# Kernel tuning notes

Hardware: AMD Instinct MI355X
Metric: run time of the kernel (lower is better)

The kernel has to match this reference:

```python
import jax, jax.numpy as jnp
import numpy as np

HEADS = 12
D_MODEL = 768
D_K = D_MODEL // HEADS


def setup_inputs() -> dict:
    key = jax.random.key(0)
    ks = jax.random.split(key, 5)
    B, S = 2, 2048
    scale = 1.0 / np.sqrt(D_MODEL)
    return {
        "q": jax.random.normal(ks[0], (B, S, D_MODEL), dtype=jnp.float32),
        "k": jax.random.normal(ks[1], (B, S, D_MODEL), dtype=jnp.float32),
        "v": jax.random.normal(ks[2], (B, S, D_MODEL), dtype=jnp.float32),
        "Wk": jax.random.normal(ks[3], (D_MODEL, D_MODEL), dtype=jnp.float32) * scale,
        "bk": jnp.zeros((D_MODEL,), dtype=jnp.float32),
        "Wo": jax.random.normal(ks[4], (D_MODEL, D_MODEL), dtype=jnp.float32) * scale,
        "bo": jnp.zeros((D_MODEL,), dtype=jnp.float32),
    }


def reference(q, k, v, Wk, bk, Wo, bo):
    B, S, _ = q.shape
    # NOTE: faithful to source bug: q, k, v ALL projected with k_linear.
    def proj(x):
        y = x @ Wk.T + bk                    # [B,S,D]
        return y.reshape(B, -1, HEADS, D_K).transpose(0, 2, 1, 3)  # [B,H,S,Dk]

    qh, kh, vh = proj(q), proj(k), proj(v)
    scores = jnp.einsum('bhsd,bhtd->bhst', qh, kh) / jnp.sqrt(jnp.float32(D_K))
    attn = jax.nn.softmax(scores, axis=-1)   # dropout is identity in eval
    out = jnp.einsum('bhst,bhtd->bhsd', attn, vh)
    concat = out.transpose(0, 2, 1, 3).reshape(B, -1, D_MODEL)
    return concat @ Wo.T + bo
```

## Files before the change

kernel.cpp:

```cpp
#include <hip/hip_runtime.h>
#include <hip/hip_bf16.h>
#include <stddef.h>

#define HEADS 12
#define DM 768
#define DK 64
#define SEQ 2048
#define NB 2
#define WSZ (DM * DM)

typedef __attribute__((ext_vector_type(8))) short short8;
typedef __attribute__((ext_vector_type(4))) float f32x4;

#define MFMA16(A, B, C) __builtin_amdgcn_mfma_f32_16x16x32_bf16((A), (B), (C), 0, 0, 0)

__device__ __forceinline__ unsigned short f2bf(float x) {
  union { float f; unsigned u; } c;
  c.f = x;
  unsigned r = (c.u + 0x7FFFu + ((c.u >> 16) & 1u)) >> 16;
  return (unsigned short)r;
}
__device__ __forceinline__ float bf2f(unsigned short h) {
  union { float f; unsigned u; } c;
  c.u = ((unsigned)h) << 16;
  return c.f;
}

__device__ __forceinline__ void async16(const void* g, void* l) {
  __builtin_amdgcn_global_load_lds(
      (const __attribute__((address_space(1))) void*)g,
      (__attribute__((address_space(3))) void*)l, 16, 0, 0);
}

__device__ __forceinline__ void splitpk(float a, float b, unsigned& hu, unsigned& lu) {
  union { __hip_bfloat162 v; unsigned u; } c;
  c.v = __float22bfloat162_rn(make_float2(a, b));
  hu = c.u;
  const float ra = a - bf2f((unsigned short)(hu & 0xFFFFu));
  const float rb = b - bf2f((unsigned short)(hu >> 16));
  c.v = __float22bfloat162_rn(make_float2(ra, rb));
  lu = c.u;
}

__device__ __forceinline__ unsigned pk2bf(float a, float b) {
  union { __hip_bfloat162 v; unsigned u; } c;
  c.v = __float22bfloat162_rn(make_float2(a, b));
  return c.u;
}

__global__ __launch_bounds__(256) void prep_split(
    const float* __restrict__ q, const float* __restrict__ k,
    const float* __restrict__ v, const float* __restrict__ Wk,
    const float* __restrict__ Wo, unsigned short* __restrict__ xq_h,
    unsigned short* __restrict__ xq_l, unsigned short* __restrict__ xk_h,
    unsigned short* __restrict__ xv_h, unsigned short* __restrict__ wkh,
    unsigned short* __restrict__ wkl, unsigned short* __restrict__ woh,
    unsigned short* __restrict__ wol) {
  const int id = blockIdx.x;
  const float* S;
  unsigned short *H, *L = nullptr;
  int base;
  if (id < 1536) { S = q; H = xq_h; L = xq_l; base = id; }
  else if (id < 3072) { S = k; H = xk_h; base = id - 1536; }
  else if (id < 4608) { S = v; H = xv_h; base = id - 3072; }
  else if (id < 4896) { S = Wk; H = wkh; L = wkl; base = id - 4608; }
  else { S = Wo; H = woh; L = wol; base = id - 4896; }

  const int i = (base * 256 + threadIdx.x) * 8;
  float a[8];
  *(float4*)&a[0] = *(const float4*)&S[i];
  *(float4*)&a[4] = *(const float4*)&S[i + 4];
  if (L) {
    unsigned hu[4], lu[4];
#pragma unroll
    for (int u = 0; u < 4; ++u) splitpk(a[2 * u], a[2 * u + 1], hu[u], lu[u]);
    *(uint4*)&H[i] = *(uint4*)&hu[0];
    *(uint4*)&L[i] = *(uint4*)&lu[0];
  } else {
    unsigned hu[4];
#pragma unroll
    for (int u = 0; u < 4; ++u) hu[u] = pk2bf(a[2 * u], a[2 * u + 1]);
    *(uint4*)&H[i] = *(uint4*)&hu[0];
  }
}

__global__ __launch_bounds__(256, 3) void gemm_proj(
    const unsigned short* __restrict__ Xh_, const unsigned short* __restrict__ Xl_,
    const unsigned short* __restrict__ Kh_, const unsigned short* __restrict__ Vh_,
    const unsigned short* __restrict__ Bh_, const unsigned short* __restrict__ Bl_,
    const float* __restrict__ bias, unsigned short* __restrict__ q_h,
    unsigned short* __restrict__ q_l, unsigned short* __restrict__ k_h,
    unsigned short* __restrict__ vt_h) {
  __shared__ __align__(16) short Ash[128 * 32];
  __shared__ __align__(16) short Asl[128 * 32];
  __shared__ __align__(16) short Bsh[96 * 32];
  __shared__ __align__(16) short Bsl[96 * 32];

  const int tid = threadIdx.x;
  const int z = blockIdx.z;
  const unsigned short* __restrict__ Ah = (z == 0) ? Xh_ : (z == 1) ? Kh_ : Vh_;
  const int id = blockIdx.x;
  const int m0 = (id & 31) << 7, n0 = (id >> 5) * 96;
  const int lane = tid & 63, wv = tid >> 6;
  const int l15 = lane & 15, quad = lane >> 4;
  const int wm = (wv >> 1) * 64, wn = (wv & 1) * 48;
  const int c0 = wv * 64 + lane, c1 = 256 + c0;
  const int b0 = (wv * 64) << 3, b1 = (256 + wv * 64) << 3;

  f32x4 acc[4][3];
#pragma unroll
  for (int i = 0; i < 4; ++i)
#pragma unroll
    for (int j = 0; j < 3; ++j) acc[i][j] = (f32x4){0.f, 0.f, 0.f, 0.f};

  for (int k0 = 0; k0 < DM; k0 += 32) {
    __syncthreads();
    async16(&Ah[(size_t)(m0 + (c0 >> 2)) * DM + k0 + (c0 & 3) * 8], &Ash[b0]);
    async16(&Ah[(size_t)(m0 + (c1 >> 2)) * DM + k0 + (c1 & 3) * 8], &Ash[b1]);
    if (z == 0) {
      async16(&Xl_[(size_t)(m0 + (c0 >> 2)) * DM + k0 + (c0 & 3) * 8], &Asl[b0]);
      async16(&Xl_[(size_t)(m0 + (c1 >> 2)) * DM + k0 + (c1 & 3) * 8], &Asl[b1]);
    }
    async16(&Bh_[(size_t)(n0 + (c0 >> 2)) * DM + k0 + (c0 & 3) * 8], &Bsh[b0]);
    async16(&Bl_[(size_t)(n0 + (c0 >> 2)) * DM + k0 + (c0 & 3) * 8], &Bsl[b0]);
    if (wv < 2) {
      async16(&Bh_[(size_t)(n0 + (c1 >> 2)) * DM + k0 + (c1 & 3) * 8], &Bsh[b1]);
      async16(&Bl_[(size_t)(n0 + (c1 >> 2)) * DM + k0 + (c1 & 3) * 8], &Bsl[b1]);
    }
    __syncthreads();

    short8 bh8[3], bl8[3];
#pragma unroll
    for (int nt = 0; nt < 3; ++nt) {
      bh8[nt] = *(const short8*)&Bsh[(wn + nt * 16 + l15) * 32 + quad * 8];
      bl8[nt] = *(const short8*)&Bsl[(wn + nt * 16 + l15) * 32 + quad * 8];
    }
#pragma unroll
    for (int mt = 0; mt < 4; ++mt) {
      const short8 ah8 = *(const short8*)&Ash[(wm + mt * 16 + l15) * 32 + quad * 8];
#pragma unroll
      for (int nt = 0; nt < 3; ++nt) {
        acc[mt][nt] = MFMA16(ah8, bh8[nt], acc[mt][nt]);
        acc[mt][nt] = MFMA16(ah8, bl8[nt], acc[mt][nt]);
      }
      if (z == 0) {
        const short8 al8 = *(const short8*)&Asl[(wm + mt * 16 + l15) * 32 + quad * 8];
#pragma unroll
        for (int nt = 0; nt < 3; ++nt) acc[mt][nt] = MFMA16(al8, bh8[nt], acc[mt][nt]);
      }
    }
  }

#pragma unroll
  for (int mt = 0; mt < 4; ++mt)
#pragma unroll
    for (int nt = 0; nt < 3; ++nt) {
      const int n = n0 + wn + nt * 16 + l15;
      const float bv = bias[n];
      const int hh = n >> 6, dk = n & 63;
#pragma unroll
      for (int j = 0; j < 4; ++j) {
        const int m = m0 + wm + mt * 16 + quad * 4 + j;
        const float y = acc[mt][nt][j] + bv;
        const int b = m >> 11, s = m & 2047;
        const unsigned short yh = f2bf(y);
        if (z == 0) {
          const int a = ((b * HEADS + hh) * SEQ + s) * DK + dk;
          q_h[a] = yh;
          q_l[a] = f2bf(y - bf2f(yh));
        } else if (z == 1) {
          k_h[((b * HEADS + hh) * SEQ + s) * DK + dk] = yh;
        } else {
          vt_h[((b * HEADS + hh) * DK + dk) * SEQ + s] = yh;
        }
      }
    }
}

__global__ __launch_bounds__(256, 2) void gemm_out(
    const unsigned short* __restrict__ Ah_, const unsigned short* __restrict__ Al_,
    const unsigned short* __restrict__ Bh_, const unsigned short* __restrict__ Bl_,
    const float* __restrict__ bias, float* __restrict__ outF) {
  __shared__ __align__(16) short Ash[64 * 32];
  __shared__ __align__(16) short Asl[64 * 32];
  __shared__ __align__(16) short Bsh[96 * 32];
  __shared__ __align__(16) short Bsl[96 * 32];

  const int tid = threadIdx.x;
  const int id = blockIdx.x;
  const int m0 = (id & 63) << 6, n0 = (id >> 6) * 96;
  const int lane = tid & 63, wv = tid >> 6;
  const int l15 = lane & 15, quad = lane >> 4;
  const int wm = (wv >> 1) * 32, wn = (wv & 1) * 48;
  const int c0 = wv * 64 + lane, c1 = 256 + c0;
  const int b0 = (wv * 64) << 3, b1 = (256 + wv * 64) << 3;

  f32x4 acc[2][3];
#pragma unroll
  for (int i = 0; i < 2; ++i)
#pragma unroll
    for (int j = 0; j < 3; ++j) acc[i][j] = (f32x4){0.f, 0.f, 0.f, 0.f};

  for (int k0 = 0; k0 < DM; k0 += 32) {
    __syncthreads();
    async16(&Ah_[(size_t)(m0 + (c0 >> 2)) * DM + k0 + (c0 & 3) * 8], &Ash[b0]);
    async16(&Al_[(size_t)(m0 + (c0 >> 2)) * DM + k0 + (c0 & 3) * 8], &Asl[b0]);
    async16(&Bh_[(size_t)(n0 + (c0 >> 2)) * DM + k0 + (c0 & 3) * 8], &Bsh[b0]);
    async16(&Bl_[(size_t)(n0 + (c0 >> 2)) * DM + k0 + (c0 & 3) * 8], &Bsl[b0]);
    if (wv < 2) {
      async16(&Bh_[(size_t)(n0 + (c1 >> 2)) * DM + k0 + (c1 & 3) * 8], &Bsh[b1]);
      async16(&Bl_[(size_t)(n0 + (c1 >> 2)) * DM + k0 + (c1 & 3) * 8], &Bsl[b1]);
    }
    __syncthreads();

    short8 bh8[3], bl8[3];
#pragma unroll
    for (int nt = 0; nt < 3; ++nt) {
      bh8[nt] = *(const short8*)&Bsh[(wn + nt * 16 + l15) * 32 + quad * 8];
      bl8[nt] = *(const short8*)&Bsl[(wn + nt * 16 + l15) * 32 + quad * 8];
    }
#pragma unroll
    for (int mt = 0; mt < 2; ++mt) {
      const short8 ah8 = *(const short8*)&Ash[(wm + mt * 16 + l15) * 32 + quad * 8];
      const short8 al8 = *(const short8*)&Asl[(wm + mt * 16 + l15) * 32 + quad * 8];
#pragma unroll
      for (int nt = 0; nt < 3; ++nt) {
        acc[mt][nt] = MFMA16(ah8, bh8[nt], acc[mt][nt]);
        acc[mt][nt] = MFMA16(al8, bh8[nt], acc[mt][nt]);
        acc[mt][nt] = MFMA16(ah8, bl8[nt], acc[mt][nt]);
      }
    }
  }

#pragma unroll
  for (int mt = 0; mt < 2; ++mt)
#pragma unroll
    for (int nt = 0; nt < 3; ++nt) {
      const int n = n0 + wn + nt * 16 + l15;
      const float bv = bias[n];
#pragma unroll
      for (int j = 0; j < 4; ++j) {
        const int m = m0 + wm + mt * 16 + quad * 4 + j;
        outF[(size_t)m * DM + n] = acc[mt][nt][j] + bv;
      }
    }
}

__global__ __launch_bounds__(256, 3) void attn_mfma(
    const unsigned short* __restrict__ q_h, const unsigned short* __restrict__ q_l,
    const unsigned short* __restrict__ k_h, const unsigned short* __restrict__ vt_h,
    unsigned short* __restrict__ cch, unsigned short* __restrict__ ccl) {
  __shared__ __align__(16) short Ks[2][64 * 32];
  __shared__ __align__(16) short Vs[2][64 * 32];
  __shared__ __align__(16) short Ps[4][32 * 40];
  __shared__ float Osh[64 * 68];
  __shared__ float Lred[4][2][16];

  const int tid = threadIdx.x, lane = tid & 63, wv = tid >> 6;
  const int l15 = lane & 15, quad = lane >> 4;
  const int qh = wv & 1, th = wv >> 1;
  const int id = blockIdx.x;
  const int bh = id % 24, q0 = (id / 24) << 6;
  const int crow = (wv * 64 + lane) >> 2, csub = (lane & 3) * 8;
  const int ldsb = (wv * 64) << 3;

  short8 Qf[2][2][2];
#pragma unroll
  for (int qt = 0; qt < 2; ++qt)
#pragma unroll
    for (int ks = 0; ks < 2; ++ks) {
      const int off =
          (bh * SEQ + q0 + qh * 32 + qt * 16 + l15) * DK + ks * 32 + quad * 8;
      Qf[qt][ks][0] = *(const short8*)&q_h[off];
      Qf[qt][ks][1] = *(const short8*)&q_l[off];
    }

  f32x4 O[2][4];
#pragma unroll
  for (int i = 0; i < 2; ++i)
#pragma unroll
    for (int j = 0; j < 4; ++j) O[i][j] = (f32x4){0.f, 0.f, 0.f, 0.f};
  float lsum[2] = {0.f, 0.f};

  const int kbase = bh * SEQ * DK;
  const int vbase = bh * DK * SEQ;

  for (int t0 = 0; t0 < SEQ; t0 += 64) {
    __syncthreads();
    async16(&k_h[kbase + (t0 + crow) * DK + csub], &Ks[0][ldsb]);
    async16(&k_h[kbase + (t0 + crow) * DK + 32 + csub], &Ks[1][ldsb]);
    async16(&vt_h[vbase + crow * SEQ + t0 + csub], &Vs[0][ldsb]);
    async16(&vt_h[vbase + crow * SEQ + t0 + 32 + csub], &Vs[1][ldsb]);
    __syncthreads();

    f32x4 St[2][2];
#pragma unroll
    for (int i = 0; i < 2; ++i)
#pragma unroll
      for (int j = 0; j < 2; ++j) St[i][j] = (f32x4){0.f, 0.f, 0.f, 0.f};
#pragma unroll
    for (int ks = 0; ks < 2; ++ks)
#pragma unroll
      for (int tt = 0; tt < 2; ++tt) {
        const short8 kh8 =
            *(const short8*)&Ks[ks][(th * 32 + tt * 16 + l15) * 32 + quad * 8];
#pragma unroll
        for (int qt = 0; qt < 2; ++qt) {
          St[tt][qt] = MFMA16(kh8, Qf[qt][ks][0], St[tt][qt]);
          St[tt][qt] = MFMA16(kh8, Qf[qt][ks][1], St[tt][qt]);
        }
      }

#pragma unroll
    for (int tt = 0; tt < 2; ++tt)
#pragma unroll
      for (int qt = 0; qt < 2; ++qt) {
        const float p0 = __expf(fminf(St[tt][qt][0] * 0.125f, 30.f));
        const float p1 = __expf(fminf(St[tt][qt][1] * 0.125f, 30.f));
        const float p2 = __expf(fminf(St[tt][qt][2] * 0.125f, 30.f));
        const float p3 = __expf(fminf(St[tt][qt][3] * 0.125f, 30.f));
        lsum[qt] += (p0 + p1) + (p2 + p3);
        unsigned pk[2];
        pk[0] = pk2bf(p0, p1);
        pk[1] = pk2bf(p2, p3);
        *(uint2*)&Ps[wv][(qt * 16 + l15) * 40 + tt * 16 + quad * 4] =
            *(uint2*)&pk[0];
      }
    asm volatile("s_waitcnt lgkmcnt(0)" ::: "memory");

    short8 pf[2];
#pragma unroll
    for (int qt = 0; qt < 2; ++qt)
      pf[qt] = *(const short8*)&Ps[wv][(qt * 16 + l15) * 40 + quad * 8];
#pragma unroll
    for (int nt = 0; nt < 4; ++nt) {
      const short8 vh8 =
          *(const short8*)&Vs[th][(nt * 16 + l15) * 32 + quad * 8];
      O[0][nt] = MFMA16(pf[0], vh8, O[0][nt]);
      O[1][nt] = MFMA16(pf[1], vh8, O[1][nt]);
    }
  }

#pragma unroll
  for (int qt = 0; qt < 2; ++qt) {
    float l = lsum[qt];
    l += __shfl_xor(l, 16);
    l += __shfl_xor(l, 32);
    if (quad == 0) Lred[wv][qt][l15] = l;
  }
  __syncthreads();
  if (th == 1) {
#pragma unroll
    for (int qt = 0; qt < 2; ++qt)
#pragma unroll
      for (int nt = 0; nt < 4; ++nt)
#pragma unroll
        for (int j = 0; j < 4; ++j)
          Osh[(qh * 32 + qt * 16 + quad * 4 + j) * 68 + nt * 16 + l15] =
              O[qt][nt][j];
  }
  __syncthreads();
  if (th == 0) {
    const int b = bh / HEADS, hh = bh % HEADS;
#pragma unroll
    for (int qt = 0; qt < 2; ++qt)
#pragma unroll
      for (int j = 0; j < 4; ++j) {
        const int qloc = qt * 16 + quad * 4 + j;
        const float inv =
            1.0f / (Lred[wv][qt][quad * 4 + j] + Lred[wv + 2][qt][quad * 4 + j]);
        const int qrow = q0 + qh * 32 + qloc;
#pragma unroll
        for (int nt = 0; nt < 4; ++nt) {
          const float y =
              (O[qt][nt][j] + Osh[(qh * 32 + qloc) * 68 + nt * 16 + l15]) * inv;
          const size_t a =
              ((size_t)b * SEQ + qrow) * DM + hh * DK + nt * 16 + l15;
          const unsigned short yh = f2bf(y);
          cch[a] = yh;
          ccl[a] = f2bf(y - bf2f(yh));
        }
      }
  }
}

extern "C" void kernel_launch(void* const* d_in, const int* in_sizes, int n_in,
                              void* d_out, int out_size, void* d_ws,
                              size_t ws_size, hipStream_t stream) {
  const float* q = (const float*)d_in[0];
  const float* k = (const float*)d_in[1];
  const float* v = (const float*)d_in[2];
  const float* Wk = (const float*)d_in[3];
  const float* bk = (const float*)d_in[4];
  const float* Wo = (const float*)d_in[5];
  const float* bo = (const float*)d_in[6];
  float* out = (float*)d_out;

  const size_t SZ = (size_t)NB * SEQ * DM;
  unsigned short* ws16 = (unsigned short*)d_ws;
  unsigned short* xq_h = ws16;
  unsigned short* xq_l = ws16 + SZ;
  unsigned short* xk_h = ws16 + 2 * SZ;
  unsigned short* xv_h = ws16 + 3 * SZ;
  unsigned short* cch = xq_h;
  unsigned short* ccl = xq_l;
  unsigned short* qp_h = ws16 + 4 * SZ;
  unsigned short* qp_l = ws16 + 5 * SZ;
  unsigned short* kp_h = ws16 + 6 * SZ;
  unsigned short* vtp_h = ws16 + 7 * SZ;
  unsigned short* wkh = ws16 + 8 * SZ;
  unsigned short* wkl = wkh + WSZ;
  unsigned short* woh = wkl + WSZ;
  unsigned short* wol = woh + WSZ;

  prep_split<<<dim3(5184), 256, 0, stream>>>(q, k, v, Wk, Wo, xq_h, xq_l, xk_h,
                                             xv_h, wkh, wkl, woh, wol);
  gemm_proj<<<dim3(256, 1, 3), 256, 0, stream>>>(xq_h, xq_l, xk_h, xv_h, wkh,
                                                 wkl, bk, qp_h, qp_l, kp_h,
                                                 vtp_h);
  attn_mfma<<<dim3(768), 256, 0, stream>>>(qp_h, qp_l, kp_h, vtp_h, cch, ccl);
  gemm_out<<<dim3(512), 256, 0, stream>>>(cch, ccl, woh, wol, bo, out);
}
```

Before: 209.2 us.

## Pre-tile all operands into MFMA fragment layout and fold softmax scale into Q

The prep kernel now transposes inputs and weights through LDS into 16x32 MFMA fragment tiles of 512 elements. Every GEMM and attention load then becomes one contiguous 1 KB block per wave, which removes strided row gathers and LDS bank conflicts. The K and V^T projections are written straight into that tiled layout, and the Q low-part term is dropped from the projection. The 1/sqrt(dk)*log2(e) scale is folded into Q so the softmax uses exp2 directly. In exchange, the index math is more complex and the Q projection loses precision from the missing low part.

```diff
diff --git a/kernel.cpp b/kernel.cpp
--- a/kernel.cpp
+++ b/kernel.cpp
@@ -8,6 +8,7 @@
 #define SEQ 2048
 #define NB 2
 #define WSZ (DM * DM)
+#define QSCALE 0.18033688011112043f
 
 typedef __attribute__((ext_vector_type(8))) short short8;
 typedef __attribute__((ext_vector_type(4))) float f32x4;
@@ -41,71 +42,92 @@
   c.v = __float22bfloat162_rn(make_float2(ra, rb));
   lu = c.u;
 }
-
 __device__ __forceinline__ unsigned pk2bf(float a, float b) {
   union { __hip_bfloat162 v; unsigned u; } c;
   c.v = __float22bfloat162_rn(make_float2(a, b));
   return c.u;
 }
 
+
 __global__ __launch_bounds__(256) void prep_split(
     const float* __restrict__ q, const float* __restrict__ k,
     const float* __restrict__ v, const float* __restrict__ Wk,
-    const float* __restrict__ Wo, unsigned short* __restrict__ xq_h,
-    unsigned short* __restrict__ xq_l, unsigned short* __restrict__ xk_h,
-    unsigned short* __restrict__ xv_h, unsigned short* __restrict__ wkh,
-    unsigned short* __restrict__ wkl, unsigned short* __restrict__ woh,
-    unsigned short* __restrict__ wol) {
-  const int id = blockIdx.x;
+    const float* __restrict__ Wo, unsigned short* __restrict__ xq,
+    unsigned short* __restrict__ xk, unsigned short* __restrict__ xv,
+    unsigned short* __restrict__ wkh, unsigned short* __restrict__ wkl,
+    unsigned short* __restrict__ woh, unsigned short* __restrict__ wol) {
+  __shared__ __align__(16) unsigned short Lh[64 * 136];
+  __shared__ __align__(16) unsigned short Ll[64 * 136];
+  const int tid = threadIdx.x;
+  int id = blockIdx.x;
   const float* S;
   unsigned short *H, *L = nullptr;
-  int base;
-  if (id < 1536) { S = q; H = xq_h; L = xq_l; base = id; }
-  else if (id < 3072) { S = k; H = xk_h; base = id - 1536; }
-  else if (id < 4608) { S = v; H = xv_h; base = id - 3072; }
-  else if (id < 4896) { S = Wk; H = wkh; L = wkl; base = id - 4608; }
-  else { S = Wo; H = woh; L = wol; base = id - 4896; }
-
-  const int i = (base * 256 + threadIdx.x) * 8;
-  float a[8];
-  *(float4*)&a[0] = *(const float4*)&S[i];
-  *(float4*)&a[4] = *(const float4*)&S[i + 4];
-  if (L) {
-    unsigned hu[4], lu[4];
-#pragma unroll
-    for (int u = 0; u < 4; ++u) splitpk(a[2 * u], a[2 * u + 1], hu[u], lu[u]);
-    *(uint4*)&H[i] = *(uint4*)&hu[0];
-    *(uint4*)&L[i] = *(uint4*)&lu[0];
+  int RT, RT16;
+  if (id < 1152) {
+    S = (id < 384) ? q : (id < 768) ? k : v;
+    H = (id < 384) ? xq : (id < 768) ? xk : xv;
+    id = id % 384; RT = 64; RT16 = 256;
+  } else if (id < 1224) {
+    S = Wk; H = wkh; L = wkl; id -= 1152; RT = 12; RT16 = 48;
   } else {
-    unsigned hu[4];
-#pragma unroll
-    for (int u = 0; u < 4; ++u) hu[u] = pk2bf(a[2 * u], a[2 * u + 1]);
-    *(uint4*)&H[i] = *(uint4*)&hu[0];
+    S = Wo; H = woh; L = wol; id -= 1224; RT = 12; RT16 = 48;
+  }
+  const int rb = id % RT, kb = id / RT;
+  const int mlane = tid >> 4;
+  const int klane = (tid & 15) * 8;
+
+#pragma unroll
+  for (int rr = 0; rr < 4; ++rr) {
+    const int m = rr * 16 + mlane;
+    const float* src = &S[(size_t)(rb * 64 + m) * DM + kb * 128 + klane];
+    float a[8];
+    *(float4*)&a[0] = *(const float4*)&src[0];
+    *(float4*)&a[4] = *(const float4*)&src[4];
+    if (L) {
+      unsigned hu[4], lu[4];
+#pragma unroll
+      for (int u = 0; u < 4; ++u) splitpk(a[2 * u], a[2 * u + 1], hu[u], lu[u]);
+      *(uint4*)&Lh[m * 136 + klane] = *(uint4*)&hu[0];
+      *(uint4*)&Ll[m * 136 + klane] = *(uint4*)&lu[0];
+    } else {
+      unsigned hu[4];
+#pragma unroll
+      for (int u = 0; u < 4; ++u) hu[u] = pk2bf(a[2 * u], a[2 * u + 1]);
+      *(uint4*)&Lh[m * 136 + klane] = *(uint4*)&hu[0];
+    }
+  }
+  __syncthreads();
+
+  const int t = tid >> 4;
+  const int ktp = t >> 2, mtp = t & 3;
+  const size_t gt = ((size_t)(kb * 4 + ktp) * RT16 + (rb * 4 + mtp)) * 512;
+#pragma unroll
+  for (int i = 0; i < 4; ++i) {
+    const int c = i * 16 + (tid & 15);
+    const int lsrc = (mtp * 16 + (tid & 15)) * 136 + ktp * 32 + i * 8;
+    *(uint4*)&H[gt + c * 8] = *(uint4*)&Lh[lsrc];
+    if (L) *(uint4*)&L[gt + c * 8] = *(uint4*)&Ll[lsrc];
   }
 }
 
 __global__ __launch_bounds__(256, 3) void gemm_proj(
-    const unsigned short* __restrict__ Xh_, const unsigned short* __restrict__ Xl_,
-    const unsigned short* __restrict__ Kh_, const unsigned short* __restrict__ Vh_,
-    const unsigned short* __restrict__ Bh_, const unsigned short* __restrict__ Bl_,
-    const float* __restrict__ bias, unsigned short* __restrict__ q_h,
-    unsigned short* __restrict__ q_l, unsigned short* __restrict__ k_h,
-    unsigned short* __restrict__ vt_h) {
-  __shared__ __align__(16) short Ash[128 * 32];
-  __shared__ __align__(16) short Asl[128 * 32];
-  __shared__ __align__(16) short Bsh[96 * 32];
-  __shared__ __align__(16) short Bsl[96 * 32];
-
-  const int tid = threadIdx.x;
-  const int z = blockIdx.z;
-  const unsigned short* __restrict__ Ah = (z == 0) ? Xh_ : (z == 1) ? Kh_ : Vh_;
+    const unsigned short* __restrict__ Xq, const unsigned short* __restrict__ Xk,
+    const unsigned short* __restrict__ Xv, const unsigned short* __restrict__ Bh_,
+    const unsigned short* __restrict__ Bl_, const float* __restrict__ bias,
+    unsigned short* __restrict__ q_h, unsigned short* __restrict__ q_l,
+    unsigned short* __restrict__ k_h, unsigned short* __restrict__ vt_h) {
+  __shared__ __align__(16) unsigned short Ash[8 * 512];
+  __shared__ __align__(16) unsigned short Bsh[6 * 512];
+  __shared__ __align__(16) unsigned short Bsl[6 * 512];
+
+  const int tid = threadIdx.x, z = blockIdx.z;
+  const unsigned short* __restrict__ A = (z == 0) ? Xq : (z == 1) ? Xk : Xv;
   const int id = blockIdx.x;
-  const int m0 = (id & 31) << 7, n0 = (id >> 5) * 96;
+  const int mt0 = (id & 31) * 8, nt0 = (id >> 5) * 6;
   const int lane = tid & 63, wv = tid >> 6;
   const int l15 = lane & 15, quad = lane >> 4;
-  const int wm = (wv >> 1) * 64, wn = (wv & 1) * 48;
-  const int c0 = wv * 64 + lane, c1 = 256 + c0;
-  const int b0 = (wv * 64) << 3, b1 = (256 + wv * 64) << 3;
+  const int wm = (wv >> 1) * 4, wn = (wv & 1) * 3;
+  const int lx = lane * 8;
 
   f32x4 acc[4][3];
 #pragma unroll
@@ -113,41 +135,32 @@
 #pragma unroll
     for (int j = 0; j < 3; ++j) acc[i][j] = (f32x4){0.f, 0.f, 0.f, 0.f};
 
-  for (int k0 = 0; k0 < DM; k0 += 32) {
-    __syncthreads();
-    async16(&Ah[(size_t)(m0 + (c0 >> 2)) * DM + k0 + (c0 & 3) * 8], &Ash[b0]);
-    async16(&Ah[(size_t)(m0 + (c1 >> 2)) * DM + k0 + (c1 & 3) * 8], &Ash[b1]);
-    if (z == 0) {
-      async16(&Xl_[(size_t)(m0 + (c0 >> 2)) * DM + k0 + (c0 & 3) * 8], &Asl[b0]);
-      async16(&Xl_[(size_t)(m0 + (c1 >> 2)) * DM + k0 + (c1 & 3) * 8], &Asl[b1]);
-    }
-    async16(&Bh_[(size_t)(n0 + (c0 >> 2)) * DM + k0 + (c0 & 3) * 8], &Bsh[b0]);
-    async16(&Bl_[(size_t)(n0 + (c0 >> 2)) * DM + k0 + (c0 & 3) * 8], &Bsl[b0]);
-    if (wv < 2) {
-      async16(&Bh_[(size_t)(n0 + (c1 >> 2)) * DM + k0 + (c1 & 3) * 8], &Bsh[b1]);
-      async16(&Bl_[(size_t)(n0 + (c1 >> 2)) * DM + k0 + (c1 & 3) * 8], &Bsl[b1]);
-    }
+  for (int kt = 0; kt < 24; ++kt) {
+    __syncthreads();
+    async16(&A[((size_t)kt * 256 + mt0 + wv) * 512 + lx], &Ash[wv * 512]);
+    async16(&A[((size_t)kt * 256 + mt0 + wv + 4) * 512 + lx], &Ash[(wv + 4) * 512]);
+    async16(&Bh_[((size_t)kt * 48 + nt0 + wv) * 512 + lx], &Bsh[wv * 512]);
+    async16(&Bl_[((size_t)kt * 48 + nt0 + wv) * 512 + lx], &Bsl[wv * 512]);
+    if (wv < 2)
+      async16(&Bh_[((size_t)kt * 48 + nt0 + 4 + wv) * 512 + lx], &Bsh[(4 + wv) * 512]);
+    else
+      async16(&Bl_[((size_t)kt * 48 + nt0 + 2 + wv) * 512 + lx], &Bsl[(2 + wv) * 512]);
     __syncthreads();
 
     short8 bh8[3], bl8[3];
 #pragma unroll
     for (int nt = 0; nt < 3; ++nt) {
-      bh8[nt] = *(const short8*)&Bsh[(wn + nt * 16 + l15) * 32 + quad * 8];
-      bl8[nt] = *(const short8*)&Bsl[(wn + nt * 16 + l15) * 32 + quad * 8];
+      bh8[nt] = *(const short8*)&Bsh[(wn + nt) * 512 + lx];
+      bl8[nt] = *(const short8*)&Bsl[(wn + nt) * 512 + lx];
     }
 #pragma unroll
     for (int mt = 0; mt < 4; ++mt) {
-      const short8 ah8 = *(const short8*)&Ash[(wm + mt * 16 + l15) * 32 + quad * 8];
+      const short8 ah8 = *(const short8*)&Ash[(wm + mt) * 512 + lx];
 #pragma unroll
       for (int nt = 0; nt < 3; ++nt) {
         acc[mt][nt] = MFMA16(ah8, bh8[nt], acc[mt][nt]);
         acc[mt][nt] = MFMA16(ah8, bl8[nt], acc[mt][nt]);
       }
-      if (z == 0) {
-        const short8 al8 = *(const short8*)&Asl[(wm + mt * 16 + l15) * 32 + quad * 8];
-#pragma unroll
-        for (int nt = 0; nt < 3; ++nt) acc[mt][nt] = MFMA16(al8, bh8[nt], acc[mt][nt]);
-      }
     }
   }
 
@@ -155,23 +168,28 @@
   for (int mt = 0; mt < 4; ++mt)
 #pragma unroll
     for (int nt = 0; nt < 3; ++nt) {
-      const int n = n0 + wn + nt * 16 + l15;
+      const int n = (nt0 + wn + nt) * 16 + l15;
       const float bv = bias[n];
       const int hh = n >> 6, dk = n & 63;
 #pragma unroll
       for (int j = 0; j < 4; ++j) {
-        const int m = m0 + wm + mt * 16 + quad * 4 + j;
-        const float y = acc[mt][nt][j] + bv;
-        const int b = m >> 11, s = m & 2047;
-        const unsigned short yh = f2bf(y);
+        const int m = (mt0 + wm + mt) * 16 + quad * 4 + j;
+        const int b = m >> 11, t = m & 2047;
+        const int bh = b * HEADS + hh;
         if (z == 0) {
-          const int a = ((b * HEADS + hh) * SEQ + s) * DK + dk;
+          const float y = (acc[mt][nt][j] + bv) * QSCALE;
+          const unsigned short yh = f2bf(y);
+          const int a = (bh * SEQ + t) * DK + dk;
           q_h[a] = yh;
           q_l[a] = f2bf(y - bf2f(yh));
         } else if (z == 1) {
-          k_h[((b * HEADS + hh) * SEQ + s) * DK + dk] = yh;
+          const int a = bh * 131072 + (dk >> 5) * 65536 + (t >> 4) * 512 +
+                        (((dk & 31) >> 3) * 16 + (t & 15)) * 8 + (dk & 7);
+          k_h[a] = f2bf(acc[mt][nt][j] + bv);
         } else {
-          vt_h[((b * HEADS + hh) * DK + dk) * SEQ + s] = yh;
+          const int a = bh * 131072 + (t >> 5) * 2048 + (dk >> 4) * 512 +
+                        (((t & 31) >> 3) * 16 + (dk & 15)) * 8 + (t & 7);
+          vt_h[a] = f2bf(acc[mt][nt][j] + bv);
         }
       }
     }
@@ -181,19 +199,17 @@
     const unsigned short* __restrict__ Ah_, const unsigned short* __restrict__ Al_,
     const unsigned short* __restrict__ Bh_, const unsigned short* __restrict__ Bl_,
     const float* __restrict__ bias, float* __restrict__ outF) {
-  __shared__ __align__(16) short Ash[64 * 32];
-  __shared__ __align__(16) short Asl[64 * 32];
-  __shared__ __align__(16) short Bsh[96 * 32];
-  __shared__ __align__(16) short Bsl[96 * 32];
-
-  const int tid = threadIdx.x;
-  const int id = blockIdx.x;
-  const int m0 = (id & 63) << 6, n0 = (id >> 6) * 96;
+  __shared__ __align__(16) unsigned short Ash[4 * 512];
+  __shared__ __align__(16) unsigned short Asl[4 * 512];
+  __shared__ __align__(16) unsigned short Bsh[6 * 512];
+  __shared__ __align__(16) unsigned short Bsl[6 * 512];
+
+  const int tid = threadIdx.x, id = blockIdx.x;
+  const int mt0 = (id & 63) * 4, nt0 = (id >> 6) * 6;
   const int lane = tid & 63, wv = tid >> 6;
   const int l15 = lane & 15, quad = lane >> 4;
-  const int wm = (wv >> 1) * 32, wn = (wv & 1) * 48;
-  const int c0 = wv * 64 + lane, c1 = 256 + c0;
-  const int b0 = (wv * 64) << 3, b1 = (256 + wv * 64) << 3;
+  const int wm = (wv >> 1) * 2, wn = (wv & 1) * 3;
+  const int lx = lane * 8;
 
   f32x4 acc[2][3];
 #pragma unroll
@@ -201,28 +217,28 @@
 #pragma unroll
     for (int j = 0; j < 3; ++j) acc[i][j] = (f32x4){0.f, 0.f, 0.f, 0.f};
 
-  for (int k0 = 0; k0 < DM; k0 += 32) {
-    __syncthreads();
-    async16(&Ah_[(size_t)(m0 + (c0 >> 2)) * DM + k0 + (c0 & 3) * 8], &Ash[b0]);
-    async16(&Al_[(size_t)(m0 + (c0 >> 2)) * DM + k0 + (c0 & 3) * 8], &Asl[b0]);
-    async16(&Bh_[(size_t)(n0 + (c0 >> 2)) * DM + k0 + (c0 & 3) * 8], &Bsh[b0]);
-    async16(&Bl_[(size_t)(n0 + (c0 >> 2)) * DM + k0 + (c0 & 3) * 8], &Bsl[b0]);
-    if (wv < 2) {
-      async16(&Bh_[(size_t)(n0 + (c1 >> 2)) * DM + k0 + (c1 & 3) * 8], &Bsh[b1]);
-      async16(&Bl_[(size_t)(n0 + (c1 >> 2)) * DM + k0 + (c1 & 3) * 8], &Bsl[b1]);
-    }
+  for (int kt = 0; kt < 24; ++kt) {
+    __syncthreads();
+    async16(&Ah_[((size_t)kt * 256 + mt0 + wv) * 512 + lx], &Ash[wv * 512]);
+    async16(&Al_[((size_t)kt * 256 + mt0 + wv) * 512 + lx], &Asl[wv * 512]);
+    async16(&Bh_[((size_t)kt * 48 + nt0 + wv) * 512 + lx], &Bsh[wv * 512]);
+    async16(&Bl_[((size_t)kt * 48 + nt0 + wv) * 512 + lx], &Bsl[wv * 512]);
+    if (wv < 2)
+      async16(&Bh_[((size_t)kt * 48 + nt0 + 4 + wv) * 512 + lx], &Bsh[(4 + wv) * 512]);
+    else
+      async16(&Bl_[((size_t)kt * 48 + nt0 + 2 + wv) * 512 + lx], &Bsl[(2 + wv) * 512]);
     __syncthreads();
 
     short8 bh8[3], bl8[3];
 #pragma unroll
     for (int nt = 0; nt < 3; ++nt) {
-      bh8[nt] = *(const short8*)&Bsh[(wn + nt * 16 + l15) * 32 + quad * 8];
-      bl8[nt] = *(const short8*)&Bsl[(wn + nt * 16 + l15) * 32 + quad * 8];
+      bh8[nt] = *(const short8*)&Bsh[(wn + nt) * 512 + lx];
+      bl8[nt] = *(const short8*)&Bsl[(wn + nt) * 512 + lx];
     }
 #pragma unroll
     for (int mt = 0; mt < 2; ++mt) {
-      const short8 ah8 = *(const short8*)&Ash[(wm + mt * 16 + l15) * 32 + quad * 8];
-      const short8 al8 = *(const short8*)&Asl[(wm + mt * 16 + l15) * 32 + quad * 8];
+      const short8 ah8 = *(const short8*)&Ash[(wm + mt) * 512 + lx];
+      const short8 al8 = *(const short8*)&Asl[(wm + mt) * 512 + lx];
 #pragma unroll
       for (int nt = 0; nt < 3; ++nt) {
         acc[mt][nt] = MFMA16(ah8, bh8[nt], acc[mt][nt]);
@@ -236,11 +252,11 @@
   for (int mt = 0; mt < 2; ++mt)
 #pragma unroll
     for (int nt = 0; nt < 3; ++nt) {
-      const int n = n0 + wn + nt * 16 + l15;
+      const int n = (nt0 + wn + nt) * 16 + l15;
       const float bv = bias[n];
 #pragma unroll
       for (int j = 0; j < 4; ++j) {
-        const int m = m0 + wm + mt * 16 + quad * 4 + j;
+        const int m = (mt0 + wm + mt) * 16 + quad * 4 + j;
         outF[(size_t)m * DM + n] = acc[mt][nt][j] + bv;
       }
     }
@@ -250,9 +266,9 @@
     const unsigned short* __restrict__ q_h, const unsigned short* __restrict__ q_l,
     const unsigned short* __restrict__ k_h, const unsigned short* __restrict__ vt_h,
     unsigned short* __restrict__ cch, unsigned short* __restrict__ ccl) {
-  __shared__ __align__(16) short Ks[2][64 * 32];
-  __shared__ __align__(16) short Vs[2][64 * 32];
-  __shared__ __align__(16) short Ps[4][32 * 40];
+  __shared__ __align__(16) unsigned short Ks[8 * 512];
+  __shared__ __align__(16) unsigned short Vs[8 * 512];
+  __shared__ __align__(16) unsigned short Ps[4 * 1024];
   __shared__ float Osh[64 * 68];
   __shared__ float Lred[4][2][16];
 
@@ -261,8 +277,7 @@
   const int qh = wv & 1, th = wv >> 1;
   const int id = blockIdx.x;
   const int bh = id % 24, q0 = (id / 24) << 6;
-  const int crow = (wv * 64 + lane) >> 2, csub = (lane & 3) * 8;
-  const int ldsb = (wv * 64) << 3;
+  const int lx = lane * 8;
 
   short8 Qf[2][2][2];
 #pragma unroll
@@ -282,15 +297,18 @@
     for (int j = 0; j < 4; ++j) O[i][j] = (f32x4){0.f, 0.f, 0.f, 0.f};
   float lsum[2] = {0.f, 0.f};
 
-  const int kbase = bh * SEQ * DK;
-  const int vbase = bh * DK * SEQ;
+  const size_t kbase = (size_t)bh * 131072;
+  const size_t vbase = (size_t)bh * 131072;
 
   for (int t0 = 0; t0 < SEQ; t0 += 64) {
     __syncthreads();
-    async16(&k_h[kbase + (t0 + crow) * DK + csub], &Ks[0][ldsb]);
-    async16(&k_h[kbase + (t0 + crow) * DK + 32 + csub], &Ks[1][ldsb]);
-    async16(&vt_h[vbase + crow * SEQ + t0 + csub], &Vs[0][ldsb]);
-    async16(&vt_h[vbase + crow * SEQ + t0 + 32 + csub], &Vs[1][ldsb]);
+    async16(&k_h[kbase + ((size_t)(t0 >> 4) + wv) * 512 + lx], &Ks[wv * 512]);
+    async16(&k_h[kbase + 65536 + ((size_t)(t0 >> 4) + wv) * 512 + lx],
+            &Ks[(4 + wv) * 512]);
+    async16(&vt_h[vbase + (size_t)(t0 >> 5) * 2048 + wv * 512 + lx],
+            &Vs[wv * 512]);
+    async16(&vt_h[vbase + ((size_t)(t0 >> 5) + 1) * 2048 + wv * 512 + lx],
+            &Vs[(4 + wv) * 512]);
     __syncthreads();
 
     f32x4 St[2][2];
@@ -302,8 +320,7 @@
     for (int ks = 0; ks < 2; ++ks)
 #pragma unroll
       for (int tt = 0; tt < 2; ++tt) {
-        const short8 kh8 =
-            *(const short8*)&Ks[ks][(th * 32 + tt * 16 + l15) * 32 + quad * 8];
+        const short8 kh8 = *(const short8*)&Ks[(ks * 4 + th * 2 + tt) * 512 + lx];
 #pragma unroll
         for (int qt = 0; qt < 2; ++qt) {
           St[tt][qt] = MFMA16(kh8, Qf[qt][ks][0], St[tt][qt]);
@@ -315,15 +332,16 @@
     for (int tt = 0; tt < 2; ++tt)
 #pragma unroll
       for (int qt = 0; qt < 2; ++qt) {
-        const float p0 = __expf(fminf(St[tt][qt][0] * 0.125f, 30.f));
-        const float p1 = __expf(fminf(St[tt][qt][1] * 0.125f, 30.f));
-        const float p2 = __expf(fminf(St[tt][qt][2] * 0.125f, 30.f));
-        const float p3 = __expf(fminf(St[tt][qt][3] * 0.125f, 30.f));
+        const float p0 = __builtin_amdgcn_exp2f(fminf(St[tt][qt][0], 40.f));
+        const float p1 = __builtin_amdgcn_exp2f(fminf(St[tt][qt][1], 40.f));
+        const float p2 = __builtin_amdgcn_exp2f(fminf(St[tt][qt][2], 40.f));
+        const float p3 = __builtin_amdgcn_exp2f(fminf(St[tt][qt][3], 40.f));
         lsum[qt] += (p0 + p1) + (p2 + p3);
         unsigned pk[2];
         pk[0] = pk2bf(p0, p1);
         pk[1] = pk2bf(p2, p3);
-        *(uint2*)&Ps[wv][(qt * 16 + l15) * 40 + tt * 16 + quad * 4] =
+        *(uint2*)&Ps[wv * 1024 + qt * 512 +
+                     ((2 * tt + (quad >> 1)) * 16 + l15) * 8 + (quad & 1) * 4] =
             *(uint2*)&pk[0];
       }
     asm volatile("s_waitcnt lgkmcnt(0)" ::: "memory");
@@ -331,11 +349,10 @@
     short8 pf[2];
 #pragma unroll
     for (int qt = 0; qt < 2; ++qt)
-      pf[qt] = *(const short8*)&Ps[wv][(qt * 16 + l15) * 40 + quad * 8];
+      pf[qt] = *(const short8*)&Ps[wv * 1024 + qt * 512 + lx];
 #pragma unroll
     for (int nt = 0; nt < 4; ++nt) {
-      const short8 vh8 =
-          *(const short8*)&Vs[th][(nt * 16 + l15) * 32 + quad * 8];
+      const short8 vh8 = *(const short8*)&Vs[(th * 4 + nt) * 512 + lx];
       O[0][nt] = MFMA16(pf[0], vh8, O[0][nt]);
       O[1][nt] = MFMA16(pf[1], vh8, O[1][nt]);
     }
@@ -366,16 +383,16 @@
     for (int qt = 0; qt < 2; ++qt)
 #pragma unroll
       for (int j = 0; j < 4; ++j) {
-        const int qloc = qt * 16 + quad * 4 + j;
-        const float inv =
-            1.0f / (Lred[wv][qt][quad * 4 + j] + Lred[wv + 2][qt][quad * 4 + j]);
-        const int qrow = q0 + qh * 32 + qloc;
+        const int qloc = qh * 32 + qt * 16 + quad * 4 + j;
+        const float inv = 1.0f / (Lred[wv][qt][quad * 4 + j] +
+                                  Lred[wv + 2][qt][quad * 4 + j]);
+        const int m = b * SEQ + q0 + qloc;
 #pragma unroll
         for (int nt = 0; nt < 4; ++nt) {
-          const float y =
-              (O[qt][nt][j] + Osh[(qh * 32 + qloc) * 68 + nt * 16 + l15]) * inv;
-          const size_t a =
-              ((size_t)b * SEQ + qrow) * DM + hh * DK + nt * 16 + l15;
+          const float y = (O[qt][nt][j] + Osh[qloc * 68 + nt * 16 + l15]) * inv;
+          const int kk = hh * 64 + nt * 16 + l15;
+          const int a = ((kk >> 5) * 256 + (m >> 4)) * 512 +
+                        (((kk & 31) >> 3) * 16 + (m & 15)) * 8 + (kk & 7);
           const unsigned short yh = f2bf(y);
           cch[a] = yh;
           ccl[a] = f2bf(y - bf2f(yh));
@@ -398,26 +415,24 @@
 
   const size_t SZ = (size_t)NB * SEQ * DM;
   unsigned short* ws16 = (unsigned short*)d_ws;
-  unsigned short* xq_h = ws16;
-  unsigned short* xq_l = ws16 + SZ;
-  unsigned short* xk_h = ws16 + 2 * SZ;
-  unsigned short* xv_h = ws16 + 3 * SZ;
-  unsigned short* cch = xq_h;
-  unsigned short* ccl = xq_l;
-  unsigned short* qp_h = ws16 + 4 * SZ;
-  unsigned short* qp_l = ws16 + 5 * SZ;
-  unsigned short* kp_h = ws16 + 6 * SZ;
-  unsigned short* vtp_h = ws16 + 7 * SZ;
-  unsigned short* wkh = ws16 + 8 * SZ;
+  unsigned short* xq = ws16;
+  unsigned short* xk = ws16 + SZ;
+  unsigned short* xv = ws16 + 2 * SZ;
+  unsigned short* cch = xq;
+  unsigned short* ccl = xk;
+  unsigned short* qp_h = ws16 + 3 * SZ;
+  unsigned short* qp_l = ws16 + 4 * SZ;
+  unsigned short* kp = ws16 + 5 * SZ;
+  unsigned short* vtp = ws16 + 6 * SZ;
+  unsigned short* wkh = ws16 + 7 * SZ;
   unsigned short* wkl = wkh + WSZ;
   unsigned short* woh = wkl + WSZ;
   unsigned short* wol = woh + WSZ;
 
-  prep_split<<<dim3(5184), 256, 0, stream>>>(q, k, v, Wk, Wo, xq_h, xq_l, xk_h,
-                                             xv_h, wkh, wkl, woh, wol);
-  gemm_proj<<<dim3(256, 1, 3), 256, 0, stream>>>(xq_h, xq_l, xk_h, xv_h, wkh,
-                                                 wkl, bk, qp_h, qp_l, kp_h,
-                                                 vtp_h);
-  attn_mfma<<<dim3(768), 256, 0, stream>>>(qp_h, qp_l, kp_h, vtp_h, cch, ccl);
+  prep_split<<<dim3(1296), 256, 0, stream>>>(q, k, v, Wk, Wo, xq, xk, xv, wkh,
+                                             wkl, woh, wol);
+  gemm_proj<<<dim3(256, 1, 3), 256, 0, stream>>>(xq, xk, xv, wkh, wkl, bk,
+                                                 qp_h, qp_l, kp, vtp);
+  attn_mfma<<<dim3(768), 256, 0, stream>>>(qp_h, qp_l, kp, vtp, cch, ccl);
   gemm_out<<<dim3(512), 256, 0, stream>>>(cch, ccl, woh, wol, bo, out);
 }
```

Result: no change. 206.0 us (-1.5%).
